# Performance work log

Measured on AMD Instinct MI355X. Metric: run time of the kernel, lower is better.

Reference implementation:

```python
import jax, jax.numpy as jnp
import numpy as np

N, E, D, A = 50000, 1_600_000, 32, 2
H1, C1, H2, C2 = 4, 16, 2, 32  # GATv2Conv(D,16,heads=4) -> 64; GATv2Conv(64,32,heads=2) -> 64


def setup_inputs() -> dict:
    key = jax.random.key(0)
    ks = jax.random.split(key, 16)

    def glorot(k, shape):
        fan = shape[0] + shape[-1]
        return jax.random.normal(k, shape, jnp.float32) * np.float32(np.sqrt(2.0 / fan))

    return {
        "x": jax.random.normal(ks[0], (N, D), jnp.float32),
        "edge_index": jax.random.randint(ks[1], (2, E), 0, N),
        "edge_attr": jax.random.normal(ks[2], (E, 2), jnp.float32),
        # GATv2 layer 1 (lin_l/lin_r with bias, lin_edge no bias, att [H,C], out bias)
        "w1_l": glorot(ks[3], (D, H1 * C1)), "b1_l": jnp.zeros((H1 * C1,), jnp.float32),
        "w1_r": glorot(ks[4], (D, H1 * C1)), "b1_r": jnp.zeros((H1 * C1,), jnp.float32),
        "w1_e": glorot(ks[5], (2, H1 * C1)),
        "att1": glorot(ks[6], (H1, C1)),
        "bias1": jnp.zeros((H1 * C1,), jnp.float32),
        # GATv2 layer 2
        "w2_l": glorot(ks[7], (H1 * C1, H2 * C2)), "b2_l": jnp.zeros((H2 * C2,), jnp.float32),
        "w2_r": glorot(ks[8], (H1 * C1, H2 * C2)), "b2_r": jnp.zeros((H2 * C2,), jnp.float32),
        "w2_e": glorot(ks[9], (2, H2 * C2)),
        "att2": glorot(ks[10], (H2, C2)),
        "bias2": jnp.zeros((H2 * C2,), jnp.float32),
        # heads
        "w_actor": glorot(ks[11], (H2 * C2, A)), "b_actor": jnp.zeros((A,), jnp.float32),
        "w_critic": glorot(ks[12], (H2 * C2, 1)), "b_critic": jnp.zeros((1,), jnp.float32),
        "log_std": jnp.zeros((A,), jnp.float32),
    }


def _gatv2(x, src, dst, eattr, Wl, bl, Wr, br, We, att, bias, H, C, n):
    # PyG GATv2Conv: message j->i with i = dst, j = src
    xl = (x @ Wl + bl).reshape(n, H, C)  # source-side transform (x_j)
    xr = (x @ Wr + br).reshape(n, H, C)  # target-side transform (x_i)
    ee = (eattr @ We).reshape(-1, H, C)  # per-edge embedding
    z = jax.nn.leaky_relu(xl[src] + xr[dst] + ee, 0.2)  # [Etot, H, C]
    logits = jnp.einsum('ehc,hc->eh', z, att)  # [Etot, H]
    # segment softmax over incoming edges of each dst node
    m = jax.ops.segment_max(logits, dst, num_segments=n)
    p = jnp.exp(logits - m[dst])
    denom = jax.ops.segment_sum(p, dst, num_segments=n)
    alpha = p / denom[dst]  # every node has a self-loop -> denom > 0
    msg = xl[src] * alpha[:, :, None]  # [Etot, H, C]
    out = jax.ops.segment_sum(msg, dst, num_segments=n)
    return out.reshape(n, H * C) + bias


def reference(x, edge_index, edge_attr,
              w1_l, b1_l, w1_r, b1_r, w1_e, att1, bias1,
              w2_l, b2_l, w2_r, b2_r, w2_e, att2, bias2,
              w_actor, b_actor, w_critic, b_critic, log_std):
    src, dst = edge_index[0], edge_index[1]
    # add_self_loops=True, fill_value='mean': self-loop edge_attr = mean of incoming edge_attr
    cnt = jax.ops.segment_sum(jnp.ones((edge_attr.shape[0],), x.dtype), dst, num_segments=N)
    sums = jax.ops.segment_sum(edge_attr, dst, num_segments=N)
    loop_attr = sums / jnp.maximum(cnt, 1.0)[:, None]
    loop = jnp.arange(N, dtype=src.dtype)
    src_f = jnp.concatenate([src, loop])
    dst_f = jnp.concatenate([dst, loop])
    ea = jnp.concatenate([edge_attr, loop_attr], axis=0)

    h = jax.nn.relu(_gatv2(x, src_f, dst_f, ea, w1_l, b1_l, w1_r, b1_r, w1_e, att1, bias1, H1, C1, N))
    h = jax.nn.relu(_gatv2(h, src_f, dst_f, ea, w2_l, b2_l, w2_r, b2_r, w2_e, att2, bias2, H2, C2, N))

    action_mean = jnp.tanh(h @ w_actor + b_actor)  # [N, A]
    value = h @ w_critic + b_critic               # [N, 1]
    std = jnp.exp(log_std)                        # [A]  (Normal(action_mean, std))
    return action_mean, std, value
```

## Files before the change

kernel.cpp:

```cpp
#include <hip/hip_runtime.h>
#include <math.h>

#define DIN   32
#define F1    64
#define F2    64

template <int K>
__device__ __forceinline__ void lin_lr_body(int bid,
        const float* __restrict__ x,
        const float* __restrict__ Wl, const float* __restrict__ bl,
        const float* __restrict__ Wr, const float* __restrict__ br,
        float* __restrict__ xl, float* __restrict__ xr, int n) {
    __shared__ float Ash[32][K + 4];
    __shared__ float Wsh[K][128];
    const int t = threadIdx.x;
    const int node0 = bid * 32;

    for (int idx = t; idx < 32 * (K / 4); idx += 256) {
        int m = idx / (K / 4), kq = idx % (K / 4);
        float4 v = make_float4(0.f, 0.f, 0.f, 0.f);
        if (node0 + m < n) v = ((const float4*)(x + (size_t)(node0 + m) * K))[kq];
        *(float4*)&Ash[m][kq * 4] = v;
    }
    for (int idx = t; idx < K * 32; idx += 256) {
        int k = idx / 32, j4 = idx % 32;
        float4 v = (j4 < 16) ? ((const float4*)(Wl + (size_t)k * 64))[j4]
                             : ((const float4*)(Wr + (size_t)k * 64))[j4 - 16];
        *(float4*)&Wsh[k][j4 * 4] = v;
    }
    __syncthreads();

    const int ty = t >> 4;
    const int tx = t & 15;
    float acc0[8], acc1[8];
#pragma unroll
    for (int j = 0; j < 8; j++) { acc0[j] = 0.f; acc1[j] = 0.f; }

#pragma unroll 4
    for (int k = 0; k < K; k++) {
        float a0 = Ash[ty * 2 + 0][k];
        float a1 = Ash[ty * 2 + 1][k];
        float4 w0 = *(const float4*)&Wsh[k][tx * 8];
        float4 w1 = *(const float4*)&Wsh[k][tx * 8 + 4];
        acc0[0] += a0 * w0.x; acc0[1] += a0 * w0.y;
        acc0[2] += a0 * w0.z; acc0[3] += a0 * w0.w;
        acc0[4] += a0 * w1.x; acc0[5] += a0 * w1.y;
        acc0[6] += a0 * w1.z; acc0[7] += a0 * w1.w;
        acc1[0] += a1 * w0.x; acc1[1] += a1 * w0.y;
        acc1[2] += a1 * w0.z; acc1[3] += a1 * w0.w;
        acc1[4] += a1 * w1.x; acc1[5] += a1 * w1.y;
        acc1[6] += a1 * w1.z; acc1[7] += a1 * w1.w;
    }

    const float* bsrc = (tx < 8) ? bl : br;
    int jb = (tx < 8) ? tx * 8 : (tx - 8) * 8;
    float4 b0 = ((const float4*)(bsrc + jb))[0];
    float4 b1 = ((const float4*)(bsrc + jb))[1];
    float* dst = (tx < 8) ? xl : xr;
#pragma unroll
    for (int m = 0; m < 2; m++) {
        int node = node0 + ty * 2 + m;
        if (node >= n) continue;
        const float* ac = (m == 0) ? acc0 : acc1;
        float4 o0, o1;
        o0.x = ac[0] + b0.x; o0.y = ac[1] + b0.y;
        o0.z = ac[2] + b0.z; o0.w = ac[3] + b0.w;
        o1.x = ac[4] + b1.x; o1.y = ac[5] + b1.y;
        o1.z = ac[6] + b1.z; o1.w = ac[7] + b1.w;
        ((float4*)(dst + (size_t)node * 64 + jb))[0] = o0;
        ((float4*)(dst + (size_t)node * 64 + jb))[1] = o1;
    }
}

__global__ __launch_bounds__(256, 2)
void fused_bcount_lin1(const int* __restrict__ dstr, int* __restrict__ cnt_mat,
                       int E, int Ec, int NB, int gridLin,
                       const float* __restrict__ x,
                       const float* __restrict__ Wl, const float* __restrict__ bl,
                       const float* __restrict__ Wr, const float* __restrict__ br,
                       float* __restrict__ xl, float* __restrict__ xr, int n) {
    __shared__ int hist[256];
    if ((int)blockIdx.x < gridLin) {
        lin_lr_body<DIN>(blockIdx.x, x, Wl, bl, Wr, br, xl, xr, n);
        return;
    }
    const int blk = blockIdx.x - gridLin;
    const int t = threadIdx.x;
    hist[t] = 0;
    __syncthreads();
    const int s0 = blk * Ec, s1 = min(E, s0 + Ec);
    for (int e = s0 + t; e < s1; e += 256)
        atomicAdd(&hist[dstr[e] >> 8], 1);
    __syncthreads();
    if (t < NB) cnt_mat[t * 256 + blk] = hist[t];
}


__global__ void scan_blocks(const int* __restrict__ cnt, int* __restrict__ partial,
                            int* __restrict__ btot, int n) {
    __shared__ int sh[256];
    int t = threadIdx.x;
    int i = blockIdx.x * 256 + t;
    int v = (i < n) ? cnt[i] : 0;
    sh[t] = v; __syncthreads();
    for (int off = 1; off < 256; off <<= 1) {
        int x = (t >= off) ? sh[t - off] : 0;
        __syncthreads();
        sh[t] += x;
        __syncthreads();
    }
    if (i < n) partial[i] = sh[t] - v;
    if (t == 255) btot[blockIdx.x] = sh[t];
}

__global__ void scan_add2(const int* __restrict__ partial, const int* __restrict__ btot,
                          int* __restrict__ out, int n) {
    __shared__ int sh[256];
    const int t = threadIdx.x, j = blockIdx.x;
    sh[t] = (t < j) ? btot[t] : 0;
    __syncthreads();
    for (int off = 128; off > 0; off >>= 1) {
        if (t < off) sh[t] += sh[t + off];
        __syncthreads();
    }
    int i = j * 256 + t;
    if (i < n) out[i] = partial[i] + sh[0];
}

__global__ __launch_bounds__(256)
void scatter_buckets(const int* __restrict__ srcr, const int* __restrict__ dstr,
                     const float* __restrict__ ea, const int* __restrict__ colbase,
                     int4* __restrict__ inter, int E, int Ec) {
    __shared__ int hist[256];
    const int blk = blockIdx.x;
    const int t = threadIdx.x;
    hist[t] = 0;
    __syncthreads();
    const int s0 = blk * Ec, s1 = min(E, s0 + Ec);
    for (int e = s0 + t; e < s1; e += 256) {
        int d = dstr[e];
        int b = d >> 8;
        int lr = atomicAdd(&hist[b], 1);
        float2 v = ((const float2*)ea)[e];
        int4 r;
        r.x = srcr[e];
        r.y = __float_as_int(v.x);
        r.z = __float_as_int(v.y);
        r.w = d;
        inter[colbase[b * 256 + blk] + lr] = r;
    }
}

__global__ __launch_bounds__(256)
void bucket_csr(const int4* __restrict__ inter, const int* __restrict__ colbase,
                int* __restrict__ row_ptr, int4* __restrict__ edges,
                int NB, int N, int E) {
    __shared__ int sh[256];
    __shared__ int cur[256];
    const int b = blockIdx.x, t = threadIdx.x;
    const int bstart = colbase[b * 256];
    const int bend = (b + 1 < NB) ? colbase[(b + 1) * 256] : E;

    sh[t] = 0;
    __syncthreads();
    for (int pos = bstart + t; pos < bend; pos += 256)
        atomicAdd(&sh[inter[pos].w & 255], 1);
    __syncthreads();
    int v = sh[t];
    __syncthreads();
    sh[t] = v; __syncthreads();
    for (int off = 1; off < 256; off <<= 1) {
        int x = (t >= off) ? sh[t - off] : 0;
        __syncthreads();
        sh[t] += x;
        __syncthreads();
    }
    int excl = sh[t] - v;
    cur[t] = excl;
    int node = b * 256 + t;
    if (node <= N) row_ptr[node] = bstart + excl;
    __syncthreads();
    for (int pos = bstart + t; pos < bend; pos += 256) {
        int4 r = inter[pos];
        int k = atomicAdd(&cur[r.w & 255], 1);
        edges[bstart + k] = r;
    }
}

__global__ __launch_bounds__(256, 2)
void lin_lr_tiled64(const float* __restrict__ x,
                    const float* __restrict__ Wl, const float* __restrict__ bl,
                    const float* __restrict__ Wr, const float* __restrict__ br,
                    float* __restrict__ xl, float* __restrict__ xr, int n) {
    lin_lr_body<F1>(blockIdx.x, x, Wl, bl, Wr, br, xl, xr, n);
}

template <int H, int C, bool FUSE_HEADS>
__global__ __launch_bounds__(256)
void gat_kernel(const float* __restrict__ xl, const float* __restrict__ xr,
                const int* __restrict__ row_ptr, const int4* __restrict__ edges,
                const float* __restrict__ We, const float* __restrict__ att,
                const float* __restrict__ bias, float* __restrict__ hout,
                const float* __restrict__ wa, const float* __restrict__ ba,
                const float* __restrict__ wc, const float* __restrict__ bc,
                const float* __restrict__ ls, float* __restrict__ pout,
                int n, int E) {
    constexpr int LPH = C / 4;
    if (FUSE_HEADS && blockIdx.x == 0 && threadIdx.x < 2)
        pout[(size_t)n * 2 + threadIdx.x] = expf(ls[threadIdx.x]);
    const int lane = threadIdx.x & 63;
    const int wid = (blockIdx.x * blockDim.x + threadIdx.x) >> 6;
    if (wid >= n) return;
    const int i = wid;
    const int g = lane >> 4;
    const int q = lane & 15;

    const float4* xl4 = (const float4*)xl;
    const float4 xri = ((const float4*)(xr + (size_t)i * 64))[q];
    const float4 we0 = ((const float4*)We)[q];
    const float4 we1 = ((const float4*)(We + 64))[q];
    float4 av = ((const float4*)att)[q];
    const float LOG2E = 1.4426950408889634f;
    av.x *= LOG2E; av.y *= LOG2E; av.z *= LOG2E; av.w *= LOG2E;

    float den = 0.f;
    float a0 = 0.f, a1 = 0.f, a2 = 0.f, a3 = 0.f;
    float s0 = 0.f, s1 = 0.f;

    const int e0 = row_ptr[i], e1 = row_ptr[i + 1];

    int4 rn0 = edges[min(e0 + g,     E - 1)];
    int4 rn1 = edges[min(e0 + 4 + g, E - 1)];
    float4 xvn0 = xl4[(rn0.x << 4) + q];
    float4 xvn1 = xl4[(rn1.x << 4) + q];

    for (int eb = e0; eb < e1; eb += 8) {
        int4 r0 = rn0, r1 = rn1;
        float4 xv0 = xvn0, xv1 = xvn1;
        int i0 = min(eb + 8 + g,  E - 1);
        int i1 = min(eb + 12 + g, E - 1);
        rn0 = edges[i0];
        rn1 = edges[i1];
        xvn0 = xl4[(rn0.x << 4) + q];
        xvn1 = xl4[(rn1.x << 4) + q];

        const bool v0 = (eb + g) < e1;
        const bool v1 = (eb + 4 + g) < e1;
        float ea00 = v0 ? __int_as_float(r0.y) : 0.f;
        float ea01 = v0 ? __int_as_float(r0.z) : 0.f;
        float ea10 = v1 ? __int_as_float(r1.y) : 0.f;
        float ea11 = v1 ? __int_as_float(r1.z) : 0.f;
        s0 += ea00 + ea10;
        s1 += ea01 + ea11;

        float y0 = xv0.x + fmaf(ea00, we0.x, fmaf(ea01, we1.x, xri.x));
        float y1 = xv0.y + fmaf(ea00, we0.y, fmaf(ea01, we1.y, xri.y));
        float y2 = xv0.z + fmaf(ea00, we0.z, fmaf(ea01, we1.z, xri.z));
        float y3 = xv0.w + fmaf(ea00, we0.w, fmaf(ea01, we1.w, xri.w));
        float u0 = xv1.x + fmaf(ea10, we0.x, fmaf(ea11, we1.x, xri.x));
        float u1 = xv1.y + fmaf(ea10, we0.y, fmaf(ea11, we1.y, xri.y));
        float u2 = xv1.z + fmaf(ea10, we0.z, fmaf(ea11, we1.z, xri.z));
        float u3 = xv1.w + fmaf(ea10, we0.w, fmaf(ea11, we1.w, xri.w));
        y0 = fmaxf(y0, 0.2f * y0); u0 = fmaxf(u0, 0.2f * u0);
        y1 = fmaxf(y1, 0.2f * y1); u1 = fmaxf(u1, 0.2f * u1);
        y2 = fmaxf(y2, 0.2f * y2); u2 = fmaxf(u2, 0.2f * u2);
        y3 = fmaxf(y3, 0.2f * y3); u3 = fmaxf(u3, 0.2f * u3);
        float l0 = fmaf(y0, av.x, fmaf(y1, av.y, fmaf(y2, av.z, y3 * av.w)));
        float l1 = fmaf(u0, av.x, fmaf(u1, av.y, fmaf(u2, av.z, u3 * av.w)));
#pragma unroll
        for (int m = 1; m < LPH; m <<= 1) {
            l0 += __shfl_xor(l0, m, 64);
            l1 += __shfl_xor(l1, m, 64);
        }
        float p0 = v0 ? exp2f(l0) : 0.f;
        float p1 = v1 ? exp2f(l1) : 0.f;
        den += p0 + p1;
        a0 = fmaf(p0, xv0.x, fmaf(p1, xv1.x, a0));
        a1 = fmaf(p0, xv0.y, fmaf(p1, xv1.y, a1));
        a2 = fmaf(p0, xv0.z, fmaf(p1, xv1.z, a2));
        a3 = fmaf(p0, xv0.w, fmaf(p1, xv1.w, a3));
    }

#pragma unroll
    for (int m = 16; m < 64; m <<= 1) {
        den += __shfl_xor(den, m, 64);
        a0 += __shfl_xor(a0, m, 64);
        a1 += __shfl_xor(a1, m, 64);
        a2 += __shfl_xor(a2, m, 64);
        a3 += __shfl_xor(a3, m, 64);
        s0 += __shfl_xor(s0, m, 64);
        s1 += __shfl_xor(s1, m, 64);
    }

    float degc = fmaxf((float)(e1 - e0), 1.0f);
    float la0 = s0 / degc, la1 = s1 / degc;
    const float4 xlv = xl4[(i << 4) + q];
    {
        float z0 = xlv.x + fmaf(la0, we0.x, fmaf(la1, we1.x, xri.x));
        float z1 = xlv.y + fmaf(la0, we0.y, fmaf(la1, we1.y, xri.y));
        float z2 = xlv.z + fmaf(la0, we0.z, fmaf(la1, we1.z, xri.z));
        float z3 = xlv.w + fmaf(la0, we0.w, fmaf(la1, we1.w, xri.w));
        z0 = fmaxf(z0, 0.2f * z0);
        z1 = fmaxf(z1, 0.2f * z1);
        z2 = fmaxf(z2, 0.2f * z2);
        z3 = fmaxf(z3, 0.2f * z3);
        float l = fmaf(z0, av.x, fmaf(z1, av.y, fmaf(z2, av.z, z3 * av.w)));
#pragma unroll
        for (int m = 1; m < LPH; m <<= 1) l += __shfl_xor(l, m, 64);
        float p = exp2f(l);
        den += p;
        a0 = fmaf(p, xlv.x, a0);
        a1 = fmaf(p, xlv.y, a1);
        a2 = fmaf(p, xlv.z, a2);
        a3 = fmaf(p, xlv.w, a3);
    }

    float rd = 1.0f / den;
    const float4 bv = ((const float4*)bias)[q];
    float4 o;
    o.x = fmaxf(fmaf(a0, rd, bv.x), 0.f);
    o.y = fmaxf(fmaf(a1, rd, bv.y), 0.f);
    o.z = fmaxf(fmaf(a2, rd, bv.z), 0.f);
    o.w = fmaxf(fmaf(a3, rd, bv.w), 0.f);

    if (!FUSE_HEADS) {
        if (g == 0) ((float4*)(hout + (size_t)i * 64))[q] = o;
    } else {
        float4 wa01 = ((const float4*)wa)[q * 2];
        float4 wa23 = ((const float4*)wa)[q * 2 + 1];
        float4 wcv  = ((const float4*)wc)[q];
        float d0 = o.x * wa01.x + o.y * wa01.z + o.z * wa23.x + o.w * wa23.z;
        float d1 = o.x * wa01.y + o.y * wa01.w + o.z * wa23.y + o.w * wa23.w;
        float d2 = o.x * wcv.x + o.y * wcv.y + o.z * wcv.z + o.w * wcv.w;
#pragma unroll
        for (int m = 1; m < 16; m <<= 1) {
            d0 += __shfl_xor(d0, m, 64);
            d1 += __shfl_xor(d1, m, 64);
            d2 += __shfl_xor(d2, m, 64);
        }
        if (lane == 0) {
            pout[(size_t)i * 2 + 0] = tanhf(d0 + ba[0]);
            pout[(size_t)i * 2 + 1] = tanhf(d1 + ba[1]);
            pout[(size_t)n * 2 + 2 + i] = d2 + bc[0];
        }
    }
}


extern "C" void kernel_launch(void* const* d_in, const int* in_sizes, int n_in,
                              void* d_out, int out_size, void* d_ws, size_t ws_size,
                              hipStream_t stream) {
    const float* x    = (const float*)d_in[0];
    const int*   ei   = (const int*)  d_in[1];
    const float* ea   = (const float*)d_in[2];
    const float* w1l  = (const float*)d_in[3];
    const float* b1l  = (const float*)d_in[4];
    const float* w1r  = (const float*)d_in[5];
    const float* b1r  = (const float*)d_in[6];
    const float* w1e  = (const float*)d_in[7];
    const float* att1 = (const float*)d_in[8];
    const float* bias1= (const float*)d_in[9];
    const float* w2l  = (const float*)d_in[10];
    const float* b2l  = (const float*)d_in[11];
    const float* w2r  = (const float*)d_in[12];
    const float* b2r  = (const float*)d_in[13];
    const float* w2e  = (const float*)d_in[14];
    const float* att2 = (const float*)d_in[15];
    const float* bias2= (const float*)d_in[16];
    const float* wa   = (const float*)d_in[17];
    const float* ba   = (const float*)d_in[18];
    const float* wc   = (const float*)d_in[19];
    const float* bc   = (const float*)d_in[20];
    const float* ls   = (const float*)d_in[21];

    const int N = in_sizes[0] / DIN;
    const int E = in_sizes[2] / 2;
    const int* srcr = ei;
    const int* dstr = ei + E;

    const int NB = (N + 255) >> 8;
    const int Ec = (E + 255) / 256;
    const int n2 = NB * 256;

    char* p = (char*)d_ws;
    auto alloc = [&](size_t bytes) -> void* {
        void* r = (void*)p;
        p += (bytes + 255) & ~(size_t)255;
        return r;
    };
    int*   cnt_mat = (int*)  alloc((size_t)n2 * 4);
    int*   partial = (int*)  alloc((size_t)n2 * 4);
    int*   btot    = (int*)  alloc(256 * 4);
    int*   colbase = (int*)  alloc((size_t)n2 * 4);
    int*   row_ptr = (int*)  alloc((size_t)(N + 1) * 4);
    int4*  edges   = (int4*) alloc((size_t)E * 16);
    float* xl      = (float*)alloc((size_t)N * F1 * 4);
    float* xr      = (float*)alloc((size_t)N * F1 * 4);
    float* h1      = (float*)alloc((size_t)N * F1 * 4);
    float* h2      = (float*)alloc((size_t)N * F2 * 4);
    int4* inter = (int4*)h1;
    (void)ws_size; (void)n_in; (void)out_size;

    const int TB = 256;
    int nbScan = (n2 + TB - 1) / TB;
    int gridGemm = (N + 31) / 32;
    int gridWave = (N + 3) / 4;

    fused_bcount_lin1<<<gridGemm + 256, TB, 0, stream>>>(
        dstr, cnt_mat, E, Ec, NB, gridGemm, x, w1l, b1l, w1r, b1r, xl, xr, N);
    scan_blocks<<<nbScan, TB, 0, stream>>>(cnt_mat, partial, btot, n2);
    scan_add2<<<nbScan, TB, 0, stream>>>(partial, btot, colbase, n2);
    scatter_buckets<<<256, TB, 0, stream>>>(srcr, dstr, ea, colbase, inter, E, Ec);
    bucket_csr<<<NB, TB, 0, stream>>>(inter, colbase, row_ptr, edges, NB, N, E);

    gat_kernel<4, 16, false><<<gridWave, TB, 0, stream>>>(
        xl, xr, row_ptr, edges, w1e, att1, bias1, h1,
        nullptr, nullptr, nullptr, nullptr, nullptr, nullptr, N, E);
    lin_lr_tiled64<<<gridGemm, TB, 0, stream>>>(h1, w2l, b2l, w2r, b2r, xl, xr, N);
    gat_kernel<2, 32, true><<<gridWave, TB, 0, stream>>>(
        xl, xr, row_ptr, edges, w2e, att2, bias2, h2,
        wa, ba, wc, bc, ls, (float*)d_out, N, E);
}
```

Before: 322.5 us.

## Compress edge records to 8 bytes with bf16 edge attrs and fold scan-add into consumers

```diff
diff --git a/kernel.cpp b/kernel.cpp
--- a/kernel.cpp
+++ b/kernel.cpp
@@ -4,6 +4,14 @@
 #define DIN   32
 #define F1    64
 #define F2    64
+
+__device__ __forceinline__ unsigned bf16pack(float a, float b) {
+    unsigned ua = __float_as_uint(a);
+    unsigned ub = __float_as_uint(b);
+    ua = (ua + 0x7FFFu + ((ua >> 16) & 1u)) >> 16;
+    ub = (ub + 0x7FFFu + ((ub >> 16) & 1u)) >> 16;
+    return ua | (ub << 16);
+}
 
 template <int K>
 __device__ __forceinline__ void lin_lr_body(int bid,
@@ -95,7 +103,6 @@
     if (t < NB) cnt_mat[t * 256 + blk] = hist[t];
 }
 
-
 __global__ void scan_blocks(const int* __restrict__ cnt, int* __restrict__ partial,
                             int* __restrict__ btot, int n) {
     __shared__ int sh[256];
@@ -113,28 +120,27 @@
     if (t == 255) btot[blockIdx.x] = sh[t];
 }
 
-__global__ void scan_add2(const int* __restrict__ partial, const int* __restrict__ btot,
-                          int* __restrict__ out, int n) {
-    __shared__ int sh[256];
-    const int t = threadIdx.x, j = blockIdx.x;
-    sh[t] = (t < j) ? btot[t] : 0;
-    __syncthreads();
-    for (int off = 128; off > 0; off >>= 1) {
-        if (t < off) sh[t] += sh[t + off];
-        __syncthreads();
-    }
-    int i = j * 256 + t;
-    if (i < n) out[i] = partial[i] + sh[0];
-}
-
 __global__ __launch_bounds__(256)
 void scatter_buckets(const int* __restrict__ srcr, const int* __restrict__ dstr,
-                     const float* __restrict__ ea, const int* __restrict__ colbase,
-                     int4* __restrict__ inter, int E, int Ec) {
+                     const float* __restrict__ ea,
+                     const int* __restrict__ partial, const int* __restrict__ btot,
+                     int2* __restrict__ inter, int E, int Ec, int NB) {
+    __shared__ int sh[256];
+    __shared__ int colsh[256];
     __shared__ int hist[256];
     const int blk = blockIdx.x;
     const int t = threadIdx.x;
+    int bv = (t < NB) ? btot[t] : 0;
+    sh[t] = bv;
     hist[t] = 0;
+    __syncthreads();
+    for (int off = 1; off < 256; off <<= 1) {
+        int x = (t >= off) ? sh[t - off] : 0;
+        __syncthreads();
+        sh[t] += x;
+        __syncthreads();
+    }
+    if (t < NB) colsh[t] = partial[t * 256 + blk] + (sh[t] - bv);
     __syncthreads();
     const int s0 = blk * Ec, s1 = min(E, s0 + Ec);
     for (int e = s0 + t; e < s1; e += 256) {
@@ -142,29 +148,44 @@
         int b = d >> 8;
         int lr = atomicAdd(&hist[b], 1);
         float2 v = ((const float2*)ea)[e];
-        int4 r;
-        r.x = srcr[e];
-        r.y = __float_as_int(v.x);
-        r.z = __float_as_int(v.y);
-        r.w = d;
-        inter[colbase[b * 256 + blk] + lr] = r;
+        int2 r;
+        r.x = srcr[e] | ((d & 255) << 24);
+        r.y = (int)bf16pack(v.x, v.y);
+        inter[colsh[b] + lr] = r;
     }
 }
 
 __global__ __launch_bounds__(256)
-void bucket_csr(const int4* __restrict__ inter, const int* __restrict__ colbase,
-                int* __restrict__ row_ptr, int4* __restrict__ edges,
+void bucket_csr(const int2* __restrict__ inter,
+                const int* __restrict__ partial, const int* __restrict__ btot,
+                int* __restrict__ row_ptr, int2* __restrict__ edges,
                 int NB, int N, int E) {
     __shared__ int sh[256];
     __shared__ int cur[256];
+    __shared__ int bnd[2];
     const int b = blockIdx.x, t = threadIdx.x;
-    const int bstart = colbase[b * 256];
-    const int bend = (b + 1 < NB) ? colbase[(b + 1) * 256] : E;
+
+    int bv = (t < NB) ? btot[t] : 0;
+    sh[t] = bv;
+    __syncthreads();
+    for (int off = 1; off < 256; off <<= 1) {
+        int x = (t >= off) ? sh[t - off] : 0;
+        __syncthreads();
+        sh[t] += x;
+        __syncthreads();
+    }
+    if (t == b) bnd[0] = partial[b * 256] + (sh[t] - bv);
+    if (t == b + 1 && t < NB) bnd[1] = partial[t * 256] + (sh[t] - bv);
+    if (b + 1 >= NB && t == 0) bnd[1] = E;
+    __syncthreads();
+    const int bstart = bnd[0], bend = bnd[1];
+
+    if (b == 0 && t < 16) { edges[E + t] = make_int2(0, 0); }
 
     sh[t] = 0;
     __syncthreads();
     for (int pos = bstart + t; pos < bend; pos += 256)
-        atomicAdd(&sh[inter[pos].w & 255], 1);
+        atomicAdd(&sh[((unsigned)inter[pos].x) >> 24], 1);
     __syncthreads();
     int v = sh[t];
     __syncthreads();
@@ -181,8 +202,9 @@
     if (node <= N) row_ptr[node] = bstart + excl;
     __syncthreads();
     for (int pos = bstart + t; pos < bend; pos += 256) {
-        int4 r = inter[pos];
-        int k = atomicAdd(&cur[r.w & 255], 1);
+        int2 r = inter[pos];
+        int k = atomicAdd(&cur[((unsigned)r.x) >> 24], 1);
+        r.x &= 0x00FFFFFF;
         edges[bstart + k] = r;
     }
 }
@@ -198,13 +220,13 @@
 template <int H, int C, bool FUSE_HEADS>
 __global__ __launch_bounds__(256)
 void gat_kernel(const float* __restrict__ xl, const float* __restrict__ xr,
-                const int* __restrict__ row_ptr, const int4* __restrict__ edges,
+                const int* __restrict__ row_ptr, const int2* __restrict__ edges,
                 const float* __restrict__ We, const float* __restrict__ att,
                 const float* __restrict__ bias, float* __restrict__ hout,
                 const float* __restrict__ wa, const float* __restrict__ ba,
                 const float* __restrict__ wc, const float* __restrict__ bc,
                 const float* __restrict__ ls, float* __restrict__ pout,
-                int n, int E) {
+                int n) {
     constexpr int LPH = C / 4;
     if (FUSE_HEADS && blockIdx.x == 0 && threadIdx.x < 2)
         pout[(size_t)n * 2 + threadIdx.x] = expf(ls[threadIdx.x]);
@@ -229,27 +251,25 @@
 
     const int e0 = row_ptr[i], e1 = row_ptr[i + 1];
 
-    int4 rn0 = edges[min(e0 + g,     E - 1)];
-    int4 rn1 = edges[min(e0 + 4 + g, E - 1)];
+    int2 rn0 = edges[e0 + g];
+    int2 rn1 = edges[e0 + 4 + g];
     float4 xvn0 = xl4[(rn0.x << 4) + q];
     float4 xvn1 = xl4[(rn1.x << 4) + q];
 
     for (int eb = e0; eb < e1; eb += 8) {
-        int4 r0 = rn0, r1 = rn1;
+        int2 r0 = rn0, r1 = rn1;
         float4 xv0 = xvn0, xv1 = xvn1;
-        int i0 = min(eb + 8 + g,  E - 1);
-        int i1 = min(eb + 12 + g, E - 1);
-        rn0 = edges[i0];
-        rn1 = edges[i1];
+        rn0 = edges[eb + 8 + g];
+        rn1 = edges[eb + 12 + g];
         xvn0 = xl4[(rn0.x << 4) + q];
         xvn1 = xl4[(rn1.x << 4) + q];
 
         const bool v0 = (eb + g) < e1;
         const bool v1 = (eb + 4 + g) < e1;
-        float ea00 = v0 ? __int_as_float(r0.y) : 0.f;
-        float ea01 = v0 ? __int_as_float(r0.z) : 0.f;
-        float ea10 = v1 ? __int_as_float(r1.y) : 0.f;
-        float ea11 = v1 ? __int_as_float(r1.z) : 0.f;
+        float ea00 = v0 ? __int_as_float(r0.y << 16) : 0.f;
+        float ea01 = v0 ? __int_as_float(r0.y & 0xFFFF0000) : 0.f;
+        float ea10 = v1 ? __int_as_float(r1.y << 16) : 0.f;
+        float ea11 = v1 ? __int_as_float(r1.y & 0xFFFF0000) : 0.f;
         s0 += ea00 + ea10;
         s1 += ea01 + ea11;
 
@@ -391,14 +411,13 @@
     int*   cnt_mat = (int*)  alloc((size_t)n2 * 4);
     int*   partial = (int*)  alloc((size_t)n2 * 4);
     int*   btot    = (int*)  alloc(256 * 4);
-    int*   colbase = (int*)  alloc((size_t)n2 * 4);
     int*   row_ptr = (int*)  alloc((size_t)(N + 1) * 4);
-    int4*  edges   = (int4*) alloc((size_t)E * 16);
+    int2*  edges   = (int2*) alloc((size_t)(E + 16) * 8);
     float* xl      = (float*)alloc((size_t)N * F1 * 4);
     float* xr      = (float*)alloc((size_t)N * F1 * 4);
     float* h1      = (float*)alloc((size_t)N * F1 * 4);
     float* h2      = (float*)alloc((size_t)N * F2 * 4);
-    int4* inter = (int4*)h1;
+    int2* inter = (int2*)h1;
     (void)ws_size; (void)n_in; (void)out_size;
 
     const int TB = 256;
@@ -409,15 +428,16 @@
     fused_bcount_lin1<<<gridGemm + 256, TB, 0, stream>>>(
         dstr, cnt_mat, E, Ec, NB, gridGemm, x, w1l, b1l, w1r, b1r, xl, xr, N);
     scan_blocks<<<nbScan, TB, 0, stream>>>(cnt_mat, partial, btot, n2);
-    scan_add2<<<nbScan, TB, 0, stream>>>(partial, btot, colbase, n2);
-    scatter_buckets<<<256, TB, 0, stream>>>(srcr, dstr, ea, colbase, inter, E, Ec);
-    bucket_csr<<<NB, TB, 0, stream>>>(inter, colbase, row_ptr, edges, NB, N, E);
+    scatter_buckets<<<256, TB, 0, stream>>>(srcr, dstr, ea, partial, btot,
+                                            inter, E, Ec, NB);
+    bucket_csr<<<NB, TB, 0, stream>>>(inter, partial, btot, row_ptr, edges,
+                                      NB, N, E);
 
     gat_kernel<4, 16, false><<<gridWave, TB, 0, stream>>>(
         xl, xr, row_ptr, edges, w1e, att1, bias1, h1,
-        nullptr, nullptr, nullptr, nullptr, nullptr, nullptr, N, E);
+        nullptr, nullptr, nullptr, nullptr, nullptr, nullptr, N);
     lin_lr_tiled64<<<gridGemm, TB, 0, stream>>>(h1, w2l, b2l, w2r, b2r, xl, xr, N);
     gat_kernel<2, 32, true><<<gridWave, TB, 0, stream>>>(
         xl, xr, row_ptr, edges, w2e, att2, bias2, h2,
-        wa, ba, wc, bc, ls, (float*)d_out, N, E);
-}
+        wa, ba, wc, bc, ls, (float*)d_out, N);
+}
```

After: 323.4 us. Within noise of the previous version (+0.3%).
